# Kernel optimization log

Hardware: AMD Instinct MI355X
Metric: run time of the kernel (lower is better)

The kernel has to match this reference:

```python
import jax, jax.numpy as jnp
import numpy as np

N_NODES = 50000
N_EDGES = 800000
IN_NODE = 128
IN_EDGE = 64
HEADS = 8
OUT_DIM = 8
HID = HEADS * OUT_DIM


def setup_inputs() -> dict:
    key = jax.random.key(0)
    ks = jax.random.split(key, 12)
    s = 1.0 / np.sqrt(IN_NODE)
    se = 1.0 / np.sqrt(IN_EDGE)
    return {
        "edge_index": jax.random.randint(ks[0], (2, N_EDGES), 0, N_NODES, dtype=jnp.int64),
        "h": jax.random.normal(ks[1], (N_NODES, IN_NODE), dtype=jnp.float32),
        "e": jax.random.normal(ks[2], (N_EDGES, IN_EDGE), dtype=jnp.float32),
        "WQ": jax.random.normal(ks[3], (IN_NODE, HID), dtype=jnp.float32) * s,
        "bQ": jnp.zeros((HID,), dtype=jnp.float32),
        "WK": jax.random.normal(ks[4], (IN_NODE, HID), dtype=jnp.float32) * s,
        "bK": jnp.zeros((HID,), dtype=jnp.float32),
        "WV": jax.random.normal(ks[5], (IN_NODE, HID), dtype=jnp.float32) * s,
        "bV": jnp.zeros((HID,), dtype=jnp.float32),
        "We": jax.random.normal(ks[6], (IN_EDGE, HID), dtype=jnp.float32) * se,
        "be": jnp.zeros((HID,), dtype=jnp.float32),
    }


def reference(edge_index, h, e, WQ, bQ, WK, bK, WV, bV, We, be):
    n = h.shape[0]
    # node projections -> [N, H, D]
    Q = (h @ WQ + bQ).reshape(-1, HEADS, OUT_DIM)
    K = (h @ WK + bK).reshape(-1, HEADS, OUT_DIM)
    V = (h @ WV + bV).reshape(-1, HEADS, OUT_DIM)
    pe = (e @ We + be).reshape(-1, HEADS, OUT_DIM)  # [E, H, D]

    src = edge_index[0]
    dst = edge_index[1]

    # per-edge attention score: K[src] * Q[dst] / sqrt(D) + proj_e
    score = (K[src] * Q[dst]) / np.sqrt(OUT_DIM) + pe  # [E, H, D]
    e_out = score
    a = jnp.exp(jnp.clip(score.sum(-1, keepdims=True), -5.0, 5.0))  # [E, H, 1]

    # scatter-sum of weighted V and scatter-mean of attention weights (by src)
    wV = jax.ops.segment_sum(V[src] * a, src, num_segments=n)       # [N, H, D]
    z_sum = jax.ops.segment_sum(a, src, num_segments=n)             # [N, H, 1]
    cnt = jax.ops.segment_sum(jnp.ones((src.shape[0],), a.dtype), src, num_segments=n)
    z = z_sum / jnp.maximum(cnt, 1.0)[:, None, None]                # scatter-mean

    h_out = wV / (z + 1e-06)
    return (h_out, e_out)
```

## Files before the change

### kernel.cpp

```cpp
#include <hip/hip_runtime.h>
#include <hip/hip_bf16.h>

typedef float  f32x2  __attribute__((ext_vector_type(2)));
typedef float  f32x4  __attribute__((ext_vector_type(4)));
typedef short  bf16x8 __attribute__((ext_vector_type(8)));

#define HEADS 8
#define HID 64
#define IN_NODE 128
#define IN_EDGE 64
#define LDSP 68

static __device__ __forceinline__ short f2bf(float f) {
    unsigned u = __builtin_bit_cast(unsigned, f);
    unsigned r = (u + 0x7FFFu + ((u >> 16) & 1u)) >> 16;
    return (short)r;
}

__global__ __launch_bounds__(256, 4) void qkv_kernel(
    const float* __restrict__ h,
    const float* __restrict__ WQ, const float* __restrict__ bQ,
    const float* __restrict__ WK, const float* __restrict__ bK,
    const float* __restrict__ WV, const float* __restrict__ bV,
    float* __restrict__ Q, float* __restrict__ K, float* __restrict__ V,
    int n_nodes)
{
    const int lane = threadIdx.x & 63;
    const int r16  = lane & 15;
    const int g4   = lane >> 4;
    const int wave   = blockIdx.x * (blockDim.x >> 6) + (threadIdx.x >> 6);
    const int nwaves = gridDim.x * (blockDim.x >> 6);
    const int mat  = blockIdx.y;

    const float* __restrict__ W  = (mat == 0) ? WQ : (mat == 1) ? WK : WV;
    const float* __restrict__ bp = (mat == 0) ? bQ : (mat == 1) ? bK : bV;
    float* __restrict__ out      = (mat == 0) ? Q  : (mat == 1) ? K  : V;

    bf16x8 bfr[4][4];
#pragma unroll
    for (int ct = 0; ct < 4; ++ct)
#pragma unroll
        for (int kc = 0; kc < 4; ++kc)
#pragma unroll
            for (int j = 0; j < 8; ++j) {
                int k = kc * 32 + g4 * 8 + j;
                bfr[ct][kc][j] = f2bf(W[k * HID + ct * 16 + r16]);
            }
    float bias[4];
#pragma unroll
    for (int ct = 0; ct < 4; ++ct) bias[ct] = bp[ct * 16 + r16];

    const int ntiles = (n_nodes + 15) >> 4;
    for (int tile = wave; tile < ntiles; tile += nwaves) {
        const int row0 = tile * 16;
        int arow = row0 + r16; if (arow > n_nodes - 1) arow = n_nodes - 1;
        const float* ap = h + (size_t)arow * IN_NODE + g4 * 8;

        bf16x8 afr[4];
#pragma unroll
        for (int kc = 0; kc < 4; ++kc) {
            f32x4 p0 = *reinterpret_cast<const f32x4*>(ap + kc * 32);
            f32x4 p1 = *reinterpret_cast<const f32x4*>(ap + kc * 32 + 4);
            afr[kc][0] = f2bf(p0.x); afr[kc][1] = f2bf(p0.y);
            afr[kc][2] = f2bf(p0.z); afr[kc][3] = f2bf(p0.w);
            afr[kc][4] = f2bf(p1.x); afr[kc][5] = f2bf(p1.y);
            afr[kc][6] = f2bf(p1.z); afr[kc][7] = f2bf(p1.w);
        }

        f32x4 acc[4] = {};
#pragma unroll
        for (int ct = 0; ct < 4; ++ct)
#pragma unroll
            for (int kc = 0; kc < 4; ++kc)
                acc[ct] = __builtin_amdgcn_mfma_f32_16x16x32_bf16(
                    afr[kc], bfr[ct][kc], acc[ct], 0, 0, 0);

#pragma unroll
        for (int ct = 0; ct < 4; ++ct)
#pragma unroll
            for (int r = 0; r < 4; ++r) {
                int orow = row0 + g4 * 4 + r;
                if (orow < n_nodes)
                    out[(size_t)orow * HID + ct * 16 + r16] = acc[ct][r] + bias[ct];
            }
    }
}

__global__ __launch_bounds__(256, 4) void edge_kernel(
    const int* __restrict__ ei, const float* __restrict__ e,
    const float* __restrict__ We, const float* __restrict__ be,
    const float* __restrict__ Q, const float* __restrict__ K,
    float* __restrict__ e_out, float* __restrict__ z_sum,
    float* __restrict__ cnt, int n_edges)
{
    const int lane = threadIdx.x & 63;
    const int wid  = threadIdx.x >> 6;
    const int r16  = lane & 15;
    const int g4   = lane >> 4;
    const int el   = lane >> 2;
    const int qg   = lane & 3;

    __shared__ float plds[4][16][LDSP];
    float (*my)[LDSP] = plds[wid];

    const int wave   = blockIdx.x * 4 + wid;
    const int nwaves = gridDim.x * 4;

    bf16x8 bfr[4][2];
#pragma unroll
    for (int ct = 0; ct < 4; ++ct)
#pragma unroll
        for (int kc = 0; kc < 2; ++kc)
#pragma unroll
            for (int j = 0; j < 8; ++j) {
                int k = kc * 32 + g4 * 8 + j;
                bfr[ct][kc][j] = f2bf(We[k * HID + ct * 16 + r16]);
            }
    float bias[4];
#pragma unroll
    for (int ct = 0; ct < 4; ++ct) bias[ct] = be[ct * 16 + r16];

    const float SC = 0.35355339059327373f;
    const int ntiles = (n_edges + 15) >> 4;
    for (int tile = wave; tile < ntiles; tile += nwaves) {
        const int e0 = tile * 16;

        int arow = e0 + r16; if (arow > n_edges - 1) arow = n_edges - 1;
        const float* ap = e + (size_t)arow * IN_EDGE + g4 * 8;
        f32x4 p0a = *reinterpret_cast<const f32x4*>(ap);
        f32x4 p1a = *reinterpret_cast<const f32x4*>(ap + 4);
        f32x4 p0b = *reinterpret_cast<const f32x4*>(ap + 32);
        f32x4 p1b = *reinterpret_cast<const f32x4*>(ap + 36);

        bf16x8 afr[2];
        afr[0][0] = f2bf(p0a.x); afr[0][1] = f2bf(p0a.y);
        afr[0][2] = f2bf(p0a.z); afr[0][3] = f2bf(p0a.w);
        afr[0][4] = f2bf(p1a.x); afr[0][5] = f2bf(p1a.y);
        afr[0][6] = f2bf(p1a.z); afr[0][7] = f2bf(p1a.w);
        afr[1][0] = f2bf(p0b.x); afr[1][1] = f2bf(p0b.y);
        afr[1][2] = f2bf(p0b.z); afr[1][3] = f2bf(p0b.w);
        afr[1][4] = f2bf(p1b.x); afr[1][5] = f2bf(p1b.y);
        afr[1][6] = f2bf(p1b.z); afr[1][7] = f2bf(p1b.w);

        f32x4 acc[4] = {};
#pragma unroll
        for (int ct = 0; ct < 4; ++ct) {
            acc[ct] = __builtin_amdgcn_mfma_f32_16x16x32_bf16(afr[0], bfr[ct][0], acc[ct], 0, 0, 0);
            acc[ct] = __builtin_amdgcn_mfma_f32_16x16x32_bf16(afr[1], bfr[ct][1], acc[ct], 0, 0, 0);
        }

#pragma unroll
        for (int ct = 0; ct < 4; ++ct)
#pragma unroll
            for (int r = 0; r < 4; ++r)
                my[g4 * 4 + r][ct * 16 + r16] = acc[ct][r] + bias[ct];

        int erow = e0 + el;
        bool valid = erow < n_edges;
        int erc = valid ? erow : n_edges - 1;
        int src = ei[erc];
        int dst = ei[n_edges + erc];

        const float* Kp = K + (size_t)src * HID + qg * 16;
        const float* Qp = Q + (size_t)dst * HID + qg * 16;
        f32x4 k0 = *reinterpret_cast<const f32x4*>(Kp);
        f32x4 k1 = *reinterpret_cast<const f32x4*>(Kp + 4);
        f32x4 k2 = *reinterpret_cast<const f32x4*>(Kp + 8);
        f32x4 k3 = *reinterpret_cast<const f32x4*>(Kp + 12);
        f32x4 q0 = *reinterpret_cast<const f32x4*>(Qp);
        f32x4 q1 = *reinterpret_cast<const f32x4*>(Qp + 4);
        f32x4 q2 = *reinterpret_cast<const f32x4*>(Qp + 8);
        f32x4 q3 = *reinterpret_cast<const f32x4*>(Qp + 12);

        asm volatile("s_waitcnt lgkmcnt(0)" ::: "memory");
        const float* mrow = &my[el][qg * 16];
        f32x4 p0 = *reinterpret_cast<const f32x4*>(mrow);
        f32x4 p1 = *reinterpret_cast<const f32x4*>(mrow + 4);
        f32x4 p2 = *reinterpret_cast<const f32x4*>(mrow + 8);
        f32x4 p3 = *reinterpret_cast<const f32x4*>(mrow + 12);

        f32x4 s0 = k0 * q0 * SC + p0;
        f32x4 s1 = k1 * q1 * SC + p1;
        f32x4 s2 = k2 * q2 * SC + p2;
        f32x4 s3 = k3 * q3 * SC + p3;

        if (valid) {
            float* op = e_out + (size_t)erow * HID + qg * 16;
            *reinterpret_cast<f32x4*>(op)      = s0;
            *reinterpret_cast<f32x4*>(op + 4)  = s1;
            *reinterpret_cast<f32x4*>(op + 8)  = s2;
            *reinterpret_cast<f32x4*>(op + 12) = s3;
        }

        float hs0 = ((s0.x + s0.y) + (s0.z + s0.w)) + ((s1.x + s1.y) + (s1.z + s1.w));
        float hs1 = ((s2.x + s2.y) + (s2.z + s2.w)) + ((s3.x + s3.y) + (s3.z + s3.w));
        float a0 = __expf(fminf(fmaxf(hs0, -5.0f), 5.0f));
        float a1 = __expf(fminf(fmaxf(hs1, -5.0f), 5.0f));
        if (valid) {
            atomicAdd(&z_sum[src * HEADS + qg * 2], a0);
            atomicAdd(&z_sum[src * HEADS + qg * 2 + 1], a1);
            if (qg == 0) atomicAdd(&cnt[src], 1.0f);
        }
    }
}

__global__ __launch_bounds__(256) void finalize_kernel(
    const float* __restrict__ V, const float* __restrict__ z_sum,
    const float* __restrict__ cnt, float* __restrict__ h_out, int total)
{
    int i = blockIdx.x * 256 + threadIdx.x;
    if (i >= total) return;
    int node = i >> 6;
    int head = (i >> 3) & 7;
    float S = z_sum[node * HEADS + head];
    float c = fmaxf(cnt[node], 1.0f);
    h_out[i] = V[i] * S / (S / c + 1e-6f);
}

extern "C" void kernel_launch(void* const* d_in, const int* in_sizes, int n_in,
                              void* d_out, int out_size, void* d_ws, size_t ws_size,
                              hipStream_t stream)
{
    const int*   ei = (const int*)d_in[0];
    const float* h  = (const float*)d_in[1];
    const float* e  = (const float*)d_in[2];
    const float* WQ = (const float*)d_in[3];
    const float* bQ = (const float*)d_in[4];
    const float* WK = (const float*)d_in[5];
    const float* bK = (const float*)d_in[6];
    const float* WV = (const float*)d_in[7];
    const float* bV = (const float*)d_in[8];
    const float* We = (const float*)d_in[9];
    const float* be = (const float*)d_in[10];

    const int n_nodes = in_sizes[1] / IN_NODE;
    const int n_edges = in_sizes[2] / IN_EDGE;

    float* out_h = (float*)d_out;
    float* out_e = out_h + (size_t)n_nodes * HID;

    float* Q     = (float*)d_ws;
    float* K     = Q + (size_t)n_nodes * HID;
    float* V     = K + (size_t)n_nodes * HID;
    float* z_sum = V + (size_t)n_nodes * HID;
    float* cnt   = z_sum + (size_t)n_nodes * HEADS;

    (void)hipMemsetAsync(z_sum, 0, (size_t)n_nodes * (HEADS + 1) * sizeof(float), stream);

    {
        dim3 grid(96, 3);
        qkv_kernel<<<grid, 256, 0, stream>>>(h, WQ, bQ, WK, bK, WV, bV,
                                             Q, K, V, n_nodes);
    }
    {
        edge_kernel<<<2048, 256, 0, stream>>>(ei, e, We, be, Q, K,
                                              out_e, z_sum, cnt, n_edges);
    }
    {
        const int total = n_nodes * HID;
        finalize_kernel<<<(total + 255) / 256, 256, 0, stream>>>(V, z_sum, cnt,
                                                                 out_h, total);
    }
}
```

Baseline: 240.6 us.

## Store Q/K as bf16 with prescaled K and process two edge tiles per iteration

The QKV kernel now writes Q and K in bf16, with the 1/sqrt(D) scale folded into K, so the random per-edge gathers of K[src] and Q[dst] move half the bytes. The edge kernel switches from grid-stride to contiguous tile ranges per wave and processes two tiles per iteration, issuing all global loads up front to overlap gather latency. It uses a double LDS buffer with padding changed to 69 and launch bounds relaxed to 3 blocks. Rounding Q/K to bf16 adds precision error to e_out and the attention weights.

```diff
diff --git a/kernel.cpp b/kernel.cpp
--- a/kernel.cpp
+++ b/kernel.cpp
@@ -1,20 +1,26 @@
 #include <hip/hip_runtime.h>
 #include <hip/hip_bf16.h>
 
-typedef float  f32x2  __attribute__((ext_vector_type(2)));
-typedef float  f32x4  __attribute__((ext_vector_type(4)));
-typedef short  bf16x8 __attribute__((ext_vector_type(8)));
+typedef float        f32x4  __attribute__((ext_vector_type(4)));
+typedef short        bf16x8 __attribute__((ext_vector_type(8)));
+typedef unsigned int u32x4  __attribute__((ext_vector_type(4)));
 
 #define HEADS 8
 #define HID 64
 #define IN_NODE 128
 #define IN_EDGE 64
-#define LDSP 68
+#define LDSP 69
 
 static __device__ __forceinline__ short f2bf(float f) {
     unsigned u = __builtin_bit_cast(unsigned, f);
     unsigned r = (u + 0x7FFFu + ((u >> 16) & 1u)) >> 16;
     return (short)r;
+}
+static __device__ __forceinline__ float bflo(unsigned u) {
+    return __builtin_bit_cast(float, u << 16);
+}
+static __device__ __forceinline__ float bfhi(unsigned u) {
+    return __builtin_bit_cast(float, u & 0xFFFF0000u);
 }
 
 __global__ __launch_bounds__(256, 4) void qkv_kernel(
@@ -22,8 +28,8 @@
     const float* __restrict__ WQ, const float* __restrict__ bQ,
     const float* __restrict__ WK, const float* __restrict__ bK,
     const float* __restrict__ WV, const float* __restrict__ bV,
-    float* __restrict__ Q, float* __restrict__ K, float* __restrict__ V,
-    int n_nodes)
+    unsigned short* __restrict__ Qb, unsigned short* __restrict__ Kb,
+    float* __restrict__ V, int n_nodes)
 {
     const int lane = threadIdx.x & 63;
     const int r16  = lane & 15;
@@ -34,7 +40,6 @@
 
     const float* __restrict__ W  = (mat == 0) ? WQ : (mat == 1) ? WK : WV;
     const float* __restrict__ bp = (mat == 0) ? bQ : (mat == 1) ? bK : bV;
-    float* __restrict__ out      = (mat == 0) ? Q  : (mat == 1) ? K  : V;
 
     bf16x8 bfr[4][4];
 #pragma unroll
@@ -50,6 +55,7 @@
 #pragma unroll
     for (int ct = 0; ct < 4; ++ct) bias[ct] = bp[ct * 16 + r16];
 
+    const float SC = 0.35355339059327373f;
     const int ntiles = (n_nodes + 15) >> 4;
     for (int tile = wave; tile < ntiles; tile += nwaves) {
         const int row0 = tile * 16;
@@ -80,18 +86,23 @@
 #pragma unroll
             for (int r = 0; r < 4; ++r) {
                 int orow = row0 + g4 * 4 + r;
-                if (orow < n_nodes)
-                    out[(size_t)orow * HID + ct * 16 + r16] = acc[ct][r] + bias[ct];
-            }
-    }
-}
-
-__global__ __launch_bounds__(256, 4) void edge_kernel(
+                if (orow < n_nodes) {
+                    float val = acc[ct][r] + bias[ct];
+                    size_t idx = (size_t)orow * HID + ct * 16 + r16;
+                    if (mat == 0)      Qb[idx] = (unsigned short)f2bf(val);
+                    else if (mat == 1) Kb[idx] = (unsigned short)f2bf(val * SC);
+                    else               V[idx]  = val;
+                }
+            }
+    }
+}
+
+__global__ __launch_bounds__(256, 3) void edge_kernel(
     const int* __restrict__ ei, const float* __restrict__ e,
     const float* __restrict__ We, const float* __restrict__ be,
-    const float* __restrict__ Q, const float* __restrict__ K,
+    const unsigned short* __restrict__ Qb, const unsigned short* __restrict__ Kb,
     float* __restrict__ e_out, float* __restrict__ z_sum,
-    float* __restrict__ cnt, int n_edges)
+    float* __restrict__ cnt, int n_edges, int tpw)
 {
     const int lane = threadIdx.x & 63;
     const int wid  = threadIdx.x >> 6;
@@ -100,11 +111,9 @@
     const int el   = lane >> 2;
     const int qg   = lane & 3;
 
-    __shared__ float plds[4][16][LDSP];
-    float (*my)[LDSP] = plds[wid];
-
-    const int wave   = blockIdx.x * 4 + wid;
-    const int nwaves = gridDim.x * 4;
+    __shared__ float plds[4][2][16][LDSP];
+
+    const int wave = blockIdx.x * 4 + wid;
 
     bf16x8 bfr[4][2];
 #pragma unroll
@@ -120,86 +129,114 @@
 #pragma unroll
     for (int ct = 0; ct < 4; ++ct) bias[ct] = be[ct * 16 + r16];
 
-    const float SC = 0.35355339059327373f;
     const int ntiles = (n_edges + 15) >> 4;
-    for (int tile = wave; tile < ntiles; tile += nwaves) {
-        const int e0 = tile * 16;
-
-        int arow = e0 + r16; if (arow > n_edges - 1) arow = n_edges - 1;
-        const float* ap = e + (size_t)arow * IN_EDGE + g4 * 8;
-        f32x4 p0a = *reinterpret_cast<const f32x4*>(ap);
-        f32x4 p1a = *reinterpret_cast<const f32x4*>(ap + 4);
-        f32x4 p0b = *reinterpret_cast<const f32x4*>(ap + 32);
-        f32x4 p1b = *reinterpret_cast<const f32x4*>(ap + 36);
-
-        bf16x8 afr[2];
-        afr[0][0] = f2bf(p0a.x); afr[0][1] = f2bf(p0a.y);
-        afr[0][2] = f2bf(p0a.z); afr[0][3] = f2bf(p0a.w);
-        afr[0][4] = f2bf(p1a.x); afr[0][5] = f2bf(p1a.y);
-        afr[0][6] = f2bf(p1a.z); afr[0][7] = f2bf(p1a.w);
-        afr[1][0] = f2bf(p0b.x); afr[1][1] = f2bf(p0b.y);
-        afr[1][2] = f2bf(p0b.z); afr[1][3] = f2bf(p0b.w);
-        afr[1][4] = f2bf(p1b.x); afr[1][5] = f2bf(p1b.y);
-        afr[1][6] = f2bf(p1b.z); afr[1][7] = f2bf(p1b.w);
-
-        f32x4 acc[4] = {};
-#pragma unroll
-        for (int ct = 0; ct < 4; ++ct) {
-            acc[ct] = __builtin_amdgcn_mfma_f32_16x16x32_bf16(afr[0], bfr[ct][0], acc[ct], 0, 0, 0);
-            acc[ct] = __builtin_amdgcn_mfma_f32_16x16x32_bf16(afr[1], bfr[ct][1], acc[ct], 0, 0, 0);
+    int t0 = wave * tpw;
+    int t1 = t0 + tpw; if (t1 > ntiles) t1 = ntiles;
+
+    for (int t = t0; t < t1; t += 2) {
+        f32x4 ev[2][4];
+        int srcs[2], dsts[2];
+        u32x4 kb[2][2], qb[2][2];
+#pragma unroll
+        for (int u = 0; u < 2; ++u) {
+            int tt = t + u; if (tt > ntiles - 1) tt = ntiles - 1;
+            int arow = tt * 16 + r16; if (arow > n_edges - 1) arow = n_edges - 1;
+            const float* ap = e + (size_t)arow * IN_EDGE + g4 * 8;
+            ev[u][0] = *reinterpret_cast<const f32x4*>(ap);
+            ev[u][1] = *reinterpret_cast<const f32x4*>(ap + 4);
+            ev[u][2] = *reinterpret_cast<const f32x4*>(ap + 32);
+            ev[u][3] = *reinterpret_cast<const f32x4*>(ap + 36);
+
+            int erc = tt * 16 + el; if (erc > n_edges - 1) erc = n_edges - 1;
+            srcs[u] = ei[erc];
+            dsts[u] = ei[n_edges + erc];
+            const unsigned int* kp = reinterpret_cast<const unsigned int*>(Kb)
+                                     + (size_t)srcs[u] * 32 + qg * 8;
+            const unsigned int* qp = reinterpret_cast<const unsigned int*>(Qb)
+                                     + (size_t)dsts[u] * 32 + qg * 8;
+            kb[u][0] = *reinterpret_cast<const u32x4*>(kp);
+            kb[u][1] = *reinterpret_cast<const u32x4*>(kp + 4);
+            qb[u][0] = *reinterpret_cast<const u32x4*>(qp);
+            qb[u][1] = *reinterpret_cast<const u32x4*>(qp + 4);
         }
 
 #pragma unroll
-        for (int ct = 0; ct < 4; ++ct)
-#pragma unroll
-            for (int r = 0; r < 4; ++r)
-                my[g4 * 4 + r][ct * 16 + r16] = acc[ct][r] + bias[ct];
-
-        int erow = e0 + el;
-        bool valid = erow < n_edges;
-        int erc = valid ? erow : n_edges - 1;
-        int src = ei[erc];
-        int dst = ei[n_edges + erc];
-
-        const float* Kp = K + (size_t)src * HID + qg * 16;
-        const float* Qp = Q + (size_t)dst * HID + qg * 16;
-        f32x4 k0 = *reinterpret_cast<const f32x4*>(Kp);
-        f32x4 k1 = *reinterpret_cast<const f32x4*>(Kp + 4);
-        f32x4 k2 = *reinterpret_cast<const f32x4*>(Kp + 8);
-        f32x4 k3 = *reinterpret_cast<const f32x4*>(Kp + 12);
-        f32x4 q0 = *reinterpret_cast<const f32x4*>(Qp);
-        f32x4 q1 = *reinterpret_cast<const f32x4*>(Qp + 4);
-        f32x4 q2 = *reinterpret_cast<const f32x4*>(Qp + 8);
-        f32x4 q3 = *reinterpret_cast<const f32x4*>(Qp + 12);
+        for (int u = 0; u < 2; ++u) {
+            bf16x8 afr[2];
+            afr[0][0] = f2bf(ev[u][0].x); afr[0][1] = f2bf(ev[u][0].y);
+            afr[0][2] = f2bf(ev[u][0].z); afr[0][3] = f2bf(ev[u][0].w);
+            afr[0][4] = f2bf(ev[u][1].x); afr[0][5] = f2bf(ev[u][1].y);
+            afr[0][6] = f2bf(ev[u][1].z); afr[0][7] = f2bf(ev[u][1].w);
+            afr[1][0] = f2bf(ev[u][2].x); afr[1][1] = f2bf(ev[u][2].y);
+            afr[1][2] = f2bf(ev[u][2].z); afr[1][3] = f2bf(ev[u][2].w);
+            afr[1][4] = f2bf(ev[u][3].x); afr[1][5] = f2bf(ev[u][3].y);
+            afr[1][6] = f2bf(ev[u][3].z); afr[1][7] = f2bf(ev[u][3].w);
+
+            f32x4 acc[4] = {};
+#pragma unroll
+            for (int ct = 0; ct < 4; ++ct) {
+                acc[ct] = __builtin_amdgcn_mfma_f32_16x16x32_bf16(afr[0], bfr[ct][0], acc[ct], 0, 0, 0);
+                acc[ct] = __builtin_amdgcn_mfma_f32_16x16x32_bf16(afr[1], bfr[ct][1], acc[ct], 0, 0, 0);
+            }
+#pragma unroll
+            for (int ct = 0; ct < 4; ++ct)
+#pragma unroll
+                for (int r = 0; r < 4; ++r)
+                    plds[wid][u][g4 * 4 + r][ct * 16 + r16] = acc[ct][r] + bias[ct];
+        }
 
         asm volatile("s_waitcnt lgkmcnt(0)" ::: "memory");
-        const float* mrow = &my[el][qg * 16];
-        f32x4 p0 = *reinterpret_cast<const f32x4*>(mrow);
-        f32x4 p1 = *reinterpret_cast<const f32x4*>(mrow + 4);
-        f32x4 p2 = *reinterpret_cast<const f32x4*>(mrow + 8);
-        f32x4 p3 = *reinterpret_cast<const f32x4*>(mrow + 12);
-
-        f32x4 s0 = k0 * q0 * SC + p0;
-        f32x4 s1 = k1 * q1 * SC + p1;
-        f32x4 s2 = k2 * q2 * SC + p2;
-        f32x4 s3 = k3 * q3 * SC + p3;
-
-        if (valid) {
-            float* op = e_out + (size_t)erow * HID + qg * 16;
-            *reinterpret_cast<f32x4*>(op)      = s0;
-            *reinterpret_cast<f32x4*>(op + 4)  = s1;
-            *reinterpret_cast<f32x4*>(op + 8)  = s2;
-            *reinterpret_cast<f32x4*>(op + 12) = s3;
-        }
-
-        float hs0 = ((s0.x + s0.y) + (s0.z + s0.w)) + ((s1.x + s1.y) + (s1.z + s1.w));
-        float hs1 = ((s2.x + s2.y) + (s2.z + s2.w)) + ((s3.x + s3.y) + (s3.z + s3.w));
-        float a0 = __expf(fminf(fmaxf(hs0, -5.0f), 5.0f));
-        float a1 = __expf(fminf(fmaxf(hs1, -5.0f), 5.0f));
-        if (valid) {
-            atomicAdd(&z_sum[src * HEADS + qg * 2], a0);
-            atomicAdd(&z_sum[src * HEADS + qg * 2 + 1], a1);
-            if (qg == 0) atomicAdd(&cnt[src], 1.0f);
+
+#pragma unroll
+        for (int u = 0; u < 2; ++u) {
+            const int tt = t + u;
+            const int erow = tt * 16 + el;
+            const bool valid = (tt < t1) && (erow < n_edges);
+
+            const float* mrow = &plds[wid][u][el][qg * 16];
+            f32x4 p0 = *reinterpret_cast<const f32x4*>(mrow);
+            f32x4 p1 = *reinterpret_cast<const f32x4*>(mrow + 4);
+            f32x4 p2 = *reinterpret_cast<const f32x4*>(mrow + 8);
+            f32x4 p3 = *reinterpret_cast<const f32x4*>(mrow + 12);
+            float pe[16];
+            pe[0]=p0.x; pe[1]=p0.y; pe[2]=p0.z; pe[3]=p0.w;
+            pe[4]=p1.x; pe[5]=p1.y; pe[6]=p1.z; pe[7]=p1.w;
+            pe[8]=p2.x; pe[9]=p2.y; pe[10]=p2.z; pe[11]=p2.w;
+            pe[12]=p3.x; pe[13]=p3.y; pe[14]=p3.z; pe[15]=p3.w;
+
+            float sc[16];
+#pragma unroll
+            for (int half = 0; half < 2; ++half)
+#pragma unroll
+                for (int w = 0; w < 4; ++w) {
+                    unsigned ku = kb[u][half][w];
+                    unsigned qu = qb[u][half][w];
+                    int c = half * 8 + 2 * w;
+                    sc[c]     = fmaf(bflo(ku), bflo(qu), pe[c]);
+                    sc[c + 1] = fmaf(bfhi(ku), bfhi(qu), pe[c + 1]);
+                }
+
+            if (valid) {
+                float* op = e_out + (size_t)erow * HID + qg * 16;
+                f32x4 s0 = {sc[0], sc[1], sc[2], sc[3]};
+                f32x4 s1 = {sc[4], sc[5], sc[6], sc[7]};
+                f32x4 s2 = {sc[8], sc[9], sc[10], sc[11]};
+                f32x4 s3 = {sc[12], sc[13], sc[14], sc[15]};
+                *reinterpret_cast<f32x4*>(op)      = s0;
+                *reinterpret_cast<f32x4*>(op + 4)  = s1;
+                *reinterpret_cast<f32x4*>(op + 8)  = s2;
+                *reinterpret_cast<f32x4*>(op + 12) = s3;
+            }
+
+            float hs0 = ((sc[0] + sc[1]) + (sc[2] + sc[3])) + ((sc[4] + sc[5]) + (sc[6] + sc[7]));
+            float hs1 = ((sc[8] + sc[9]) + (sc[10] + sc[11])) + ((sc[12] + sc[13]) + (sc[14] + sc[15]));
+            float a0 = __expf(fminf(fmaxf(hs0, -5.0f), 5.0f));
+            float a1 = __expf(fminf(fmaxf(hs1, -5.0f), 5.0f));
+            if (valid) {
+                atomicAdd(&z_sum[srcs[u] * HEADS + qg * 2], a0);
+                atomicAdd(&z_sum[srcs[u] * HEADS + qg * 2 + 1], a1);
+                if (qg == 0) atomicAdd(&cnt[srcs[u]], 1.0f);
+            }
         }
     }
 }
@@ -239,9 +276,9 @@
     float* out_h = (float*)d_out;
     float* out_e = out_h + (size_t)n_nodes * HID;
 
-    float* Q     = (float*)d_ws;
-    float* K     = Q + (size_t)n_nodes * HID;
-    float* V     = K + (size_t)n_nodes * HID;
+    unsigned short* Qb = (unsigned short*)d_ws;
+    unsigned short* Kb = Qb + (size_t)n_nodes * HID;
+    float* V     = (float*)(Kb + (size_t)n_nodes * HID);
     float* z_sum = V + (size_t)n_nodes * HID;
     float* cnt   = z_sum + (size_t)n_nodes * HEADS;
 
@@ -250,11 +287,15 @@
     {
         dim3 grid(96, 3);
         qkv_kernel<<<grid, 256, 0, stream>>>(h, WQ, bQ, WK, bK, WV, bV,
-                                             Q, K, V, n_nodes);
+                                             Qb, Kb, V, n_nodes);
     }
     {
-        edge_kernel<<<2048, 256, 0, stream>>>(ei, e, We, be, Q, K,
-                                              out_e, z_sum, cnt, n_edges);
+        const int nblk = 2500;
+        const int nwaves = nblk * 4;
+        const int ntiles = (n_edges + 15) >> 4;
+        const int tpw = (ntiles + nwaves - 1) / nwaves;
+        edge_kernel<<<nblk, 256, 0, stream>>>(ei, e, We, be, Qb, Kb,
+                                              out_e, z_sum, cnt, n_edges, tpw);
     }
     {
         const int total = n_nodes * HID;
```

Result: faster. 222.3 us (-7.6%).
